# Performance work log

Hardware: AMD Instinct MI355X
Metric: run time of the kernel (lower is better)

## Reference

```python
import jax, jax.numpy as jnp
import numpy as np

N = 20000
E = 320000
IN_DIM = 256
OUT_DIM = 64
HEADS = 4
EDGE_DIM = 32
NEG_SLOPE = 0.2


def setup_inputs() -> dict:
    key = jax.random.key(0)
    ks = jax.random.split(key, 10)
    HD = HEADS * OUT_DIM
    x = jax.random.normal(ks[0], (N, IN_DIM), dtype=jnp.float32)
    edge_index = jax.random.randint(ks[1], (2, E), 0, N, dtype=jnp.int64)
    edge_attr = jax.random.normal(ks[2], (E, EDGE_DIM), dtype=jnp.float32)
    # xavier_uniform with gain sqrt(2)
    def xavier(k, shape):
        fan_in, fan_out = shape[1], shape[0]
        a = np.sqrt(2.0) * np.sqrt(6.0 / (fan_in + fan_out))
        return jax.random.uniform(k, shape, jnp.float32, -a, a)
    lin_W = xavier(ks[3], (HD, IN_DIM))          # [H*D, in_dim]
    att_src = xavier(ks[4], (HEADS, OUT_DIM))    # [H, D]
    att_dst = xavier(ks[5], (HEADS, OUT_DIM))
    lin_edge_W = xavier(ks[6], (HD, EDGE_DIM))
    att_edge = xavier(ks[7], (HEADS, OUT_DIM))
    bias = jnp.zeros((HD,), dtype=jnp.float32)
    return {"x": x, "edge_index": edge_index, "edge_attr": edge_attr,
            "lin_W": lin_W, "att_src": att_src, "att_dst": att_dst,
            "lin_edge_W": lin_edge_W, "att_edge": att_edge, "bias": bias}


def _gat_forward(x, edge_attr, lin_W, att_src, att_dst, lin_edge_W, att_edge, bias, edge_index):
    n = x.shape[0]
    # add self loops (static shapes)
    loops = jnp.arange(n, dtype=edge_index.dtype)
    ei = jnp.concatenate([edge_index, jnp.stack([loops, loops])], axis=1)  # [2, E+N]
    ea = jnp.concatenate([edge_attr, jnp.zeros((n, edge_attr.shape[1]), edge_attr.dtype)], axis=0)
    src, dst = ei[0], ei[1]
    # node projection: [N, H, D]
    x_proj = (x @ lin_W.T).reshape(n, HEADS, OUT_DIM)
    # per-node attention scores, then gather scalars per edge (avoids gathering x_dst)
    s_src = jnp.einsum('nhd,hd->nh', x_proj, att_src)  # [N, H]
    s_dst = jnp.einsum('nhd,hd->nh', x_proj, att_dst)
    att = s_src[src] + s_dst[dst]                      # [E', H]
    # edge feature contribution
    e_proj = (ea @ lin_edge_W.T).reshape(-1, HEADS, OUT_DIM)
    att = att + jnp.einsum('ehd,hd->eh', e_proj, att_edge)
    att = jnp.where(att >= 0, att, NEG_SLOPE * att)    # leaky_relu
    # segment softmax over dst (self-loops guarantee every node has >=1 edge)
    seg_max = jax.ops.segment_max(att, dst, num_segments=n)
    exps = jnp.exp(att - seg_max[dst])
    denom = jax.ops.segment_sum(exps, dst, num_segments=n)
    alpha = exps / (denom[dst] + 1e-12)               # [E', H]
    # messages and scatter-sum
    m = x_proj[src] * alpha[:, :, None]               # [E', H, D]
    out = jax.ops.segment_sum(m, dst, num_segments=n) # [N, H, D]
    out = out.reshape(n, HEADS * OUT_DIM) + bias
    return out


def reference(x, edge_index, edge_attr, lin_W, att_src, att_dst, lin_edge_W, att_edge, bias):
    return _gat_forward(x, edge_attr, lin_W, att_src, att_dst, lin_edge_W, att_edge, bias, edge_index)
```

## Files before the change

kernel.cpp:

```cpp
#include <hip/hip_runtime.h>
#include <math.h>

#define IN_DIM 256
#define HD 256
#define EDGE_DIM 32
#define NEG_SLOPE 0.2f
#define NTHR 256
#define WCVT_VBS 32

typedef _Float16 f16x8 __attribute__((ext_vector_type(8)));
typedef _Float16 f16x4 __attribute__((ext_vector_type(4)));
typedef float f32x4 __attribute__((ext_vector_type(4)));

__device__ __forceinline__ f16x8 cvt8(const float* p) {
    float4 lo = *(const float4*)p;
    float4 hi = *(const float4*)(p + 4);
    auto a = __builtin_amdgcn_cvt_pkrtz(lo.x, lo.y);
    auto b = __builtin_amdgcn_cvt_pkrtz(lo.z, lo.w);
    auto c = __builtin_amdgcn_cvt_pkrtz(hi.x, hi.y);
    auto d = __builtin_amdgcn_cvt_pkrtz(hi.z, hi.w);
    f16x8 r;
    r[0] = (_Float16)a[0]; r[1] = (_Float16)a[1];
    r[2] = (_Float16)b[0]; r[3] = (_Float16)b[1];
    r[4] = (_Float16)c[0]; r[5] = (_Float16)c[1];
    r[6] = (_Float16)d[0]; r[7] = (_Float16)d[1];
    return r;
}

__device__ __forceinline__ int detect64(const int* __restrict__ ei) {
    __shared__ int anynz;
    if (threadIdx.x == 0) anynz = 0;
    __syncthreads();
    if (ei[2 * threadIdx.x + 1] != 0) atomicOr(&anynz, 1);
    __syncthreads();
    return anynz == 0;
}

__device__ __forceinline__ void load_edge(const int* ei, int e, int E, int n, int is64,
                                          int& s, int& d) {
    if (e < E) {
        if (is64) { s = ei[2 * e]; d = ei[2 * E + 2 * e]; }
        else      { s = ei[e];     d = ei[E + e]; }
    } else {
        s = d = e - E;
    }
}

__global__ __launch_bounds__(NTHR) void k_pre(const float* __restrict__ lew,
                                              const float* __restrict__ ae,
                                              const float* __restrict__ W,
                                              float* __restrict__ weff,
                                              _Float16* __restrict__ Whr,
                                              int* __restrict__ deg, int n4) {
    int b = blockIdx.x;
    int t = threadIdx.x;
    if (b == 0) {
        if (t < 128) {
            int h = t >> 5, k = t & 31;
            float s = 0.f;
#pragma unroll 8
            for (int d = 0; d < 64; ++d) s += lew[(h * 64 + d) * 32 + k] * ae[h * 64 + d];
            weff[t] = s;
        }
    } else if (b <= WCVT_VBS) {
        int idx = (b - 1) * 2048 + t * 8;
        int col = idx >> 8;
        int k = idx & 255;
        f16x8 v = cvt8(&W[idx]);
        *(f16x8*)&Whr[(size_t)(k >> 3) * 2048 + col * 8] = v;
    } else {
        int i = (b - 1 - WCVT_VBS) * 1024 + t * 4;
        if (i < n4) *(int4*)&deg[i] = make_int4(0, 0, 0, 0);
    }
}

__global__ __launch_bounds__(NTHR) void k_hist(const int* __restrict__ ei,
                                               int* __restrict__ deg,
                                               int* __restrict__ perm, int E) {
    int is64 = detect64(ei);
    int e0 = (blockIdx.x * NTHR + threadIdx.x) * 4;
    if (e0 >= E) return;
    if (e0 + 4 <= E) {
        int4 pm;
        if (!is64) {
            int4 d4 = *(const int4*)&ei[E + e0];
            pm.x = atomicAdd(&deg[d4.x], 1);
            pm.y = atomicAdd(&deg[d4.y], 1);
            pm.z = atomicAdd(&deg[d4.z], 1);
            pm.w = atomicAdd(&deg[d4.w], 1);
        } else {
            int4 a = *(const int4*)&ei[2 * E + 2 * e0];
            int4 b4 = *(const int4*)&ei[2 * E + 2 * e0 + 4];
            pm.x = atomicAdd(&deg[a.x], 1);
            pm.y = atomicAdd(&deg[a.z], 1);
            pm.z = atomicAdd(&deg[b4.x], 1);
            pm.w = atomicAdd(&deg[b4.z], 1);
        }
        *(int4*)&perm[e0] = pm;
    } else {
        for (int e = e0; e < E && e < e0 + 4; ++e) {
            int d = is64 ? ei[2 * E + 2 * e] : ei[E + e];
            perm[e] = atomicAdd(&deg[d], 1);
        }
    }
}

#define XPLN 33
__global__ __launch_bounds__(NTHR) void k_proj(const float* __restrict__ x,
                                               const _Float16* __restrict__ Whr,
                                               const float* __restrict__ asrc_g,
                                               const float* __restrict__ adst_g,
                                               _Float16* __restrict__ xph,
                                               float* __restrict__ s_src,
                                               float* __restrict__ s_dst, int n) {
    __shared__ _Float16 xs[32 * XPLN * 8];
    int t = threadIdx.x;
    int lane = t & 63;
    int w = t >> 6;
    int m0 = blockIdx.x * 32;
    int c0 = w * 64;
    int r = lane & 15;
    int kq = lane >> 4;

    {
        int rr = t >> 3;
        int kc = (t & 7) * 32;
        int grow = m0 + rr;
        if (grow < n) {
            const float* xp = &x[(size_t)grow * IN_DIM + kc];
#pragma unroll
            for (int c4 = 0; c4 < 4; ++c4) {
                f16x8 v = cvt8(xp + c4 * 8);
                *(f16x8*)&xs[(size_t)((kc >> 3) + c4) * (XPLN * 8) + rr * 8] = v;
            }
        } else {
            f16x8 z = {0, 0, 0, 0, 0, 0, 0, 0};
#pragma unroll
            for (int c4 = 0; c4 < 4; ++c4)
                *(f16x8*)&xs[(size_t)((kc >> 3) + c4) * (XPLN * 8) + rr * 8] = z;
        }
    }

    float asr[4], ads[4];
#pragma unroll
    for (int ci = 0; ci < 4; ++ci) {
        asr[ci] = asrc_g[c0 + ci * 16 + r];
        ads[ci] = adst_g[c0 + ci * 16 + r];
    }

    f32x4 acc[2][4];
#pragma unroll
    for (int mi = 0; mi < 2; ++mi)
#pragma unroll
        for (int j = 0; j < 4; ++j) acc[mi][j] = (f32x4){0.f, 0.f, 0.f, 0.f};

    __syncthreads();

#pragma unroll
    for (int k0 = 0; k0 < IN_DIM; k0 += 32) {
        int p = (k0 >> 3) + kq;
        f16x8 a0 = *(const f16x8*)&xs[(size_t)p * (XPLN * 8) + (0 * 16 + r) * 8];
        f16x8 a1 = *(const f16x8*)&xs[(size_t)p * (XPLN * 8) + (1 * 16 + r) * 8];
        f16x8 bfr[4];
#pragma unroll
        for (int ci = 0; ci < 4; ++ci)
            bfr[ci] = *(const f16x8*)&Whr[(size_t)p * 2048 + (c0 + ci * 16 + r) * 8];
#pragma unroll
        for (int ci = 0; ci < 4; ++ci) {
            acc[0][ci] = __builtin_amdgcn_mfma_f32_16x16x32_f16(a0, bfr[ci], acc[0][ci],
                                                                0, 0, 0);
            acc[1][ci] = __builtin_amdgcn_mfma_f32_16x16x32_f16(a1, bfr[ci], acc[1][ci],
                                                                0, 0, 0);
        }
    }
#pragma unroll
    for (int mi = 0; mi < 2; ++mi) {
#pragma unroll
        for (int j = 0; j < 4; ++j) {
            int orow = m0 + mi * 16 + kq * 4 + j;
            if (orow < n) {
#pragma unroll
                for (int ci = 0; ci < 4; ++ci)
                    xph[(size_t)orow * HD + c0 + ci * 16 + r] = (_Float16)acc[mi][ci][j];
            }
        }
    }
#pragma unroll
    for (int mi = 0; mi < 2; ++mi) {
#pragma unroll
        for (int j = 0; j < 4; ++j) {
            float vs = 0.f, vd = 0.f;
#pragma unroll
            for (int ci = 0; ci < 4; ++ci) {
                vs += acc[mi][ci][j] * asr[ci];
                vd += acc[mi][ci][j] * ads[ci];
            }
#pragma unroll
            for (int msk = 1; msk < 16; msk <<= 1) {
                vs += __shfl_xor(vs, msk);
                vd += __shfl_xor(vd, msk);
            }
            int orow = m0 + mi * 16 + kq * 4 + j;
            if (r == 0 && orow < n) {
                s_src[orow * 4 + w] = vs;
                s_dst[orow * 4 + w] = vd;
            }
        }
    }
}

#define SCAN_T 1024
__global__ __launch_bounds__(SCAN_T) void scan_kernel(const int* __restrict__ deg,
                                                      int* __restrict__ rowptr, int n) {
    __shared__ int sdata[SCAN_T];
    int t = threadIdx.x;
    int per = (n + SCAN_T - 1) / SCAN_T;
    int begin = t * per;
    int endi = begin + per;
    if (endi > n) endi = n;
    if (begin > n) begin = n;
    bool vec = ((begin & 3) == 0) && (((endi - begin) & 3) == 0);
    int s = 0;
    if (vec) {
        for (int i = begin; i < endi; i += 4) {
            int4 v = *(const int4*)&deg[i];
            s += v.x + v.y + v.z + v.w + 4;
        }
    } else {
        for (int i = begin; i < endi; ++i) s += deg[i] + 1;
    }
    sdata[t] = s;
    __syncthreads();
    for (int off = 1; off < SCAN_T; off <<= 1) {
        int v = 0;
        if (t >= off) v = sdata[t - off];
        __syncthreads();
        sdata[t] += v;
        __syncthreads();
    }
    int run = (t == 0) ? 0 : sdata[t - 1];
    if (vec) {
        for (int i = begin; i < endi; i += 4) {
            int4 v = *(const int4*)&deg[i];
            int4 o;
            o.x = run; run += v.x + 1;
            o.y = run; run += v.y + 1;
            o.z = run; run += v.z + 1;
            o.w = run; run += v.w + 1;
            *(int4*)&rowptr[i] = o;
        }
    } else {
        for (int i = begin; i < endi; ++i) {
            rowptr[i] = run;
            run += deg[i] + 1;
        }
    }
    if (t == SCAN_T - 1) rowptr[n] = run;
}

__global__ __launch_bounds__(NTHR) void edge_kernel(const int* __restrict__ ei,
                                                    const float* __restrict__ ea,
                                                    const float* __restrict__ s_src,
                                                    const float* __restrict__ s_dst,
                                                    const float* __restrict__ weff,
                                                    const int* __restrict__ rowptr,
                                                    const int* __restrict__ perm,
                                                    char* __restrict__ rec,
                                                    int E, int n) {
    int is64 = detect64(ei);
    __shared__ float we[128];
    if (threadIdx.x < 128) we[threadIdx.x] = weff[threadIdx.x];
    __syncthreads();
    int e = blockIdx.x * blockDim.x + threadIdx.x;
    int EP = E + n;
    if (e >= EP) return;
    int s, d;
    load_edge(ei, e, E, n, is64, s, d);
    int pos;
    if (e < E) pos = rowptr[d] + perm[e];
    else       pos = rowptr[d + 1] - 1;
    float4 vs = *(const float4*)&s_src[(size_t)s * 4];
    float4 vd = *(const float4*)&s_dst[(size_t)d * 4];
    float ed[4] = {0.f, 0.f, 0.f, 0.f};
    if (e < E) {
#pragma unroll
        for (int k = 0; k < EDGE_DIM; k += 4) {
            float4 v = *(const float4*)&ea[(size_t)e * EDGE_DIM + k];
#pragma unroll
            for (int h = 0; h < 4; ++h) {
                ed[h] += v.x * we[h * 32 + k + 0] + v.y * we[h * 32 + k + 1] +
                         v.z * we[h * 32 + k + 2] + v.w * we[h * 32 + k + 3];
            }
        }
    }
    float t0 = vs.x + vd.x + ed[0];
    float t1 = vs.y + vd.y + ed[1];
    float t2 = vs.z + vd.z + ed[2];
    float t3 = vs.w + vd.w + ed[3];
    t0 = t0 >= 0.f ? t0 : NEG_SLOPE * t0;
    t1 = t1 >= 0.f ? t1 : NEG_SLOPE * t1;
    t2 = t2 >= 0.f ? t2 : NEG_SLOPE * t2;
    t3 = t3 >= 0.f ? t3 : NEG_SLOPE * t3;
    float4 o;
    o.x = __expf(t0);
    o.y = __expf(t1);
    o.z = __expf(t2);
    o.w = __expf(t3);
    char* rp = rec + (size_t)pos * 32;
    *(int4*)rp = make_int4(s, 0, 0, 0);
    *(float4*)(rp + 16) = o;
}

__global__ __launch_bounds__(NTHR) void agg_kernel(const int* __restrict__ rowptr,
                                                   const char* __restrict__ rec,
                                                   const _Float16* __restrict__ xph,
                                                   const float* __restrict__ bias,
                                                   float* __restrict__ out, int n) {
    int wid = (blockIdx.x * blockDim.x + threadIdx.x) >> 6;
    int lane = threadIdx.x & 63;
    if (wid >= n) return;
    int sub = lane >> 5;
    int l = lane & 31;
    int h = l >> 3;
    int start = rowptr[wid];
    int end = rowptr[wid + 1];

    float dh = 0.f;
    float acc[8];
#pragma unroll
    for (int k = 0; k < 8; ++k) acc[k] = 0.f;

    int i = start;
    for (; i + 4 <= end; i += 4) {
        const char* rp0 = rec + (size_t)(i + sub) * 32;
        const char* rp1 = rec + (size_t)(i + 2 + sub) * 32;
        int s0 = *(const int*)rp0;
        int s1 = *(const int*)rp1;
        float p0 = *(const float*)(rp0 + 16 + h * 4);
        float p1 = *(const float*)(rp1 + 16 + h * 4);
        f16x8 x0 = *(const f16x8*)&xph[(size_t)s0 * HD + l * 8];
        f16x8 x1 = *(const f16x8*)&xph[(size_t)s1 * HD + l * 8];
        dh += p0 + p1;
#pragma unroll
        for (int k = 0; k < 8; ++k)
            acc[k] += p0 * (float)x0[k] + p1 * (float)x1[k];
    }
    for (; i + 2 <= end; i += 2) {
        const char* rp0 = rec + (size_t)(i + sub) * 32;
        int s0 = *(const int*)rp0;
        float p0 = *(const float*)(rp0 + 16 + h * 4);
        f16x8 x0 = *(const f16x8*)&xph[(size_t)s0 * HD + l * 8];
        dh += p0;
#pragma unroll
        for (int k = 0; k < 8; ++k) acc[k] += p0 * (float)x0[k];
    }
    if (i < end && sub == 0) {
        const char* rp0 = rec + (size_t)i * 32;
        int s0 = *(const int*)rp0;
        float p0 = *(const float*)(rp0 + 16 + h * 4);
        f16x8 x0 = *(const f16x8*)&xph[(size_t)s0 * HD + l * 8];
        dh += p0;
#pragma unroll
        for (int k = 0; k < 8; ++k) acc[k] += p0 * (float)x0[k];
    }
    dh += __shfl_xor(dh, 32);
#pragma unroll
    for (int k = 0; k < 8; ++k) acc[k] += __shfl_xor(acc[k], 32);
    float invh = 1.f / (dh + 1e-12f);
    float a0 = sub ? acc[4] : acc[0];
    float a1 = sub ? acc[5] : acc[1];
    float a2 = sub ? acc[6] : acc[2];
    float a3 = sub ? acc[7] : acc[3];
    int doff = l * 8 + sub * 4;
    float4 b = *(const float4*)&bias[doff];
    float4 o4;
    o4.x = a0 * invh + b.x;
    o4.y = a1 * invh + b.y;
    o4.z = a2 * invh + b.z;
    o4.w = a3 * invh + b.w;
    *(float4*)&out[(size_t)wid * HD + doff] = o4;
}

extern "C" void kernel_launch(void* const* d_in, const int* in_sizes, int n_in,
                              void* d_out, int out_size, void* d_ws, size_t ws_size,
                              hipStream_t stream) {
    const float* x        = (const float*)d_in[0];
    const int*   ei       = (const int*)d_in[1];
    const float* ea       = (const float*)d_in[2];
    const float* lin_W    = (const float*)d_in[3];
    const float* att_src  = (const float*)d_in[4];
    const float* att_dst  = (const float*)d_in[5];
    const float* lin_eW   = (const float*)d_in[6];
    const float* att_edge = (const float*)d_in[7];
    const float* bias     = (const float*)d_in[8];
    float* out = (float*)d_out;

    int n  = in_sizes[0] / IN_DIM;
    int E  = in_sizes[2] / EDGE_DIM;
    int EP = E + n;

    char* p = (char*)d_ws;
    auto alloc = [&](size_t bytes) {
        char* r = p;
        p += (bytes + 255) & ~(size_t)255;
        return r;
    };
    _Float16* xph   = (_Float16*)alloc((size_t)n * HD * 2);
    _Float16* Whr   = (_Float16*)alloc((size_t)HD * IN_DIM * 2);
    float* s_src    = (float*)alloc((size_t)n * 4 * 4);
    float* s_dst    = (float*)alloc((size_t)n * 4 * 4);
    char*  rec      = (char*)alloc((size_t)EP * 32);
    float* weff     = (float*)alloc(128 * 4);
    int*   deg      = (int*)alloc((size_t)(n + 4) * 4);
    int*   rowptr   = (int*)alloc((size_t)(n + 1) * 4);
    int*   perm     = (int*)alloc((size_t)E * 4);

    int n4 = (n + 3) & ~3;
    int ZV = (n4 + 1023) / 1024;

    k_pre<<<1 + WCVT_VBS + ZV, NTHR, 0, stream>>>(lin_eW, att_edge, lin_W, weff, Whr,
                                                  deg, n4);
    k_hist<<<(E + 1023) / 1024, NTHR, 0, stream>>>(ei, deg, perm, E);
    k_proj<<<(n + 31) / 32, NTHR, 0, stream>>>(x, Whr, att_src, att_dst, xph,
                                               s_src, s_dst, n);
    scan_kernel<<<1, SCAN_T, 0, stream>>>(deg, rowptr, n);
    edge_kernel<<<(EP + NTHR - 1) / NTHR, NTHR, 0, stream>>>(ei, ea, s_src, s_dst, weff,
                                                             rowptr, perm, rec, E, n);
    agg_kernel<<<(n + 3) / 4, NTHR, 0, stream>>>(rowptr, rec, xph, bias, out, n);
}
```

Before: 93.73 us.

## Pack edge records to 16 bytes with bf16 weights and stage in LDS

Edge records shrink from 32 to 16 bytes by storing the four exp attention weights as bf16 pairs next to the source index. The aggregation kernel loads each node's records (up to 64) into shared memory with one coalesced load per wave, then reads them from LDS, with a global-memory fallback for higher-degree nodes. This halves record write and read traffic and replaces scattered per-edge global loads. The cost is bf16 rounding of unnormalized weights, which lowers precision, plus a block-wide barrier.

```diff
diff --git a/kernel.cpp b/kernel.cpp
--- a/kernel.cpp
+++ b/kernel.cpp
@@ -25,6 +25,14 @@
     r[4] = (_Float16)c[0]; r[5] = (_Float16)c[1];
     r[6] = (_Float16)d[0]; r[7] = (_Float16)d[1];
     return r;
+}
+
+__device__ __forceinline__ int pack_bf16x2(float a, float b) {
+    unsigned ua = __builtin_bit_cast(unsigned, a);
+    unsigned ub = __builtin_bit_cast(unsigned, b);
+    ua = (ua + 0x7fffu + ((ua >> 16) & 1u)) >> 16;
+    ub = (ub + 0x7fffu + ((ub >> 16) & 1u)) >> 16;
+    return (int)(ua | (ub << 16));
 }
 
 __device__ __forceinline__ int detect64(const int* __restrict__ ei) {
@@ -265,7 +273,7 @@
                                                     const float* __restrict__ weff,
                                                     const int* __restrict__ rowptr,
                                                     const int* __restrict__ perm,
-                                                    char* __restrict__ rec,
+                                                    int4* __restrict__ rec,
                                                     int E, int n) {
     int is64 = detect64(ei);
     __shared__ float we[128];
@@ -301,64 +309,74 @@
     t1 = t1 >= 0.f ? t1 : NEG_SLOPE * t1;
     t2 = t2 >= 0.f ? t2 : NEG_SLOPE * t2;
     t3 = t3 >= 0.f ? t3 : NEG_SLOPE * t3;
-    float4 o;
-    o.x = __expf(t0);
-    o.y = __expf(t1);
-    o.z = __expf(t2);
-    o.w = __expf(t3);
-    char* rp = rec + (size_t)pos * 32;
-    *(int4*)rp = make_int4(s, 0, 0, 0);
-    *(float4*)(rp + 16) = o;
-}
-
+    int4 r4;
+    r4.x = s;
+    r4.y = 0;
+    r4.z = pack_bf16x2(__expf(t0), __expf(t1));
+    r4.w = pack_bf16x2(__expf(t2), __expf(t3));
+    rec[pos] = r4;
+}
+
+#define AGG_CAP 64
+__device__ __forceinline__ float rec_p(const int4& r, int h) {
+    unsigned u = (unsigned)((h < 2) ? r.z : r.w);
+    unsigned bits = (h & 1) ? (u & 0xffff0000u) : (u << 16);
+    return __builtin_bit_cast(float, bits);
+}
 __global__ __launch_bounds__(NTHR) void agg_kernel(const int* __restrict__ rowptr,
-                                                   const char* __restrict__ rec,
+                                                   const int4* __restrict__ rec,
                                                    const _Float16* __restrict__ xph,
                                                    const float* __restrict__ bias,
                                                    float* __restrict__ out, int n) {
-    int wid = (blockIdx.x * blockDim.x + threadIdx.x) >> 6;
+    __shared__ int4 rl[4][AGG_CAP];
+    int wv = threadIdx.x >> 6;
+    int wid = (blockIdx.x * NTHR + threadIdx.x) >> 6;
     int lane = threadIdx.x & 63;
+    int start = 0, end = 0, deg = 0;
+    if (wid < n) {
+        start = rowptr[wid];
+        end = rowptr[wid + 1];
+        deg = end - start;
+        if (lane < deg && lane < AGG_CAP) rl[wv][lane] = rec[start + lane];
+    }
+    __syncthreads();
     if (wid >= n) return;
     int sub = lane >> 5;
     int l = lane & 31;
     int h = l >> 3;
-    int start = rowptr[wid];
-    int end = rowptr[wid + 1];
 
     float dh = 0.f;
     float acc[8];
 #pragma unroll
     for (int k = 0; k < 8; ++k) acc[k] = 0.f;
 
-    int i = start;
-    for (; i + 4 <= end; i += 4) {
-        const char* rp0 = rec + (size_t)(i + sub) * 32;
-        const char* rp1 = rec + (size_t)(i + 2 + sub) * 32;
-        int s0 = *(const int*)rp0;
-        int s1 = *(const int*)rp1;
-        float p0 = *(const float*)(rp0 + 16 + h * 4);
-        float p1 = *(const float*)(rp1 + 16 + h * 4);
-        f16x8 x0 = *(const f16x8*)&xph[(size_t)s0 * HD + l * 8];
-        f16x8 x1 = *(const f16x8*)&xph[(size_t)s1 * HD + l * 8];
+    int stop = deg < AGG_CAP ? deg : AGG_CAP;
+    int idx = sub;
+    while (idx + 2 < stop) {
+        int4 r0 = rl[wv][idx];
+        int4 r1 = rl[wv][idx + 2];
+        float p0 = rec_p(r0, h);
+        float p1 = rec_p(r1, h);
+        f16x8 x0 = *(const f16x8*)&xph[(size_t)r0.x * HD + l * 8];
+        f16x8 x1 = *(const f16x8*)&xph[(size_t)r1.x * HD + l * 8];
         dh += p0 + p1;
 #pragma unroll
         for (int k = 0; k < 8; ++k)
             acc[k] += p0 * (float)x0[k] + p1 * (float)x1[k];
-    }
-    for (; i + 2 <= end; i += 2) {
-        const char* rp0 = rec + (size_t)(i + sub) * 32;
-        int s0 = *(const int*)rp0;
-        float p0 = *(const float*)(rp0 + 16 + h * 4);
-        f16x8 x0 = *(const f16x8*)&xph[(size_t)s0 * HD + l * 8];
+        idx += 4;
+    }
+    if (idx < stop) {
+        int4 r0 = rl[wv][idx];
+        float p0 = rec_p(r0, h);
+        f16x8 x0 = *(const f16x8*)&xph[(size_t)r0.x * HD + l * 8];
         dh += p0;
 #pragma unroll
         for (int k = 0; k < 8; ++k) acc[k] += p0 * (float)x0[k];
     }
-    if (i < end && sub == 0) {
-        const char* rp0 = rec + (size_t)i * 32;
-        int s0 = *(const int*)rp0;
-        float p0 = *(const float*)(rp0 + 16 + h * 4);
-        f16x8 x0 = *(const f16x8*)&xph[(size_t)s0 * HD + l * 8];
+    for (int j = AGG_CAP + sub; j < deg; j += 2) {
+        int4 r0 = rec[start + j];
+        float p0 = rec_p(r0, h);
+        f16x8 x0 = *(const f16x8*)&xph[(size_t)r0.x * HD + l * 8];
         dh += p0;
 #pragma unroll
         for (int k = 0; k < 8; ++k) acc[k] += p0 * (float)x0[k];
@@ -409,7 +427,7 @@
     _Float16* Whr   = (_Float16*)alloc((size_t)HD * IN_DIM * 2);
     float* s_src    = (float*)alloc((size_t)n * 4 * 4);
     float* s_dst    = (float*)alloc((size_t)n * 4 * 4);
-    char*  rec      = (char*)alloc((size_t)EP * 32);
+    int4*  rec      = (int4*)alloc((size_t)EP * 16);
     float* weff     = (float*)alloc(128 * 4);
     int*   deg      = (int*)alloc((size_t)(n + 4) * 4);
     int*   rowptr   = (int*)alloc((size_t)(n + 1) * 4);
```

After: 89.93 us. 1.04x faster.
